# Performance work log

Measured on AMD Instinct MI355X. Metric: run time of the kernel, lower is better.

The kernel has to match this reference:

```python
import jax, jax.numpy as jnp
import numpy as np

N, D, E = 50000, 128, 100000
H1, H2, H3 = 8, 8, 4
NEG_SLOPE = 0.2  # PyG GATv2Conv default negative_slope


def _gatv2_layer(x, src, dst, Wl, Wr, att, b, heads):
    # GATv2Conv(in=D, out=D, heads=heads, concat=False), share_weights=False
    C = Wl.shape[1] // heads
    xl = (x @ Wl).reshape(-1, heads, C)  # source-side transform (x_j)
    xr = (x @ Wr).reshape(-1, heads, C)  # target-side transform (x_i)
    m = jax.nn.leaky_relu(xl[src] + xr[dst], NEG_SLOPE)      # [E,H,C]
    e = jnp.einsum('ehc,hc->eh', m, att)                      # [E,H]
    # segment softmax over incoming edges of each destination node
    emax = jax.ops.segment_max(e, dst, num_segments=N)        # [N,H]
    a = jnp.exp(e - emax[dst])
    denom = jax.ops.segment_sum(a, dst, num_segments=N)       # [N,H] (>0: self-loops)
    a = a / denom[dst]
    out = jax.ops.segment_sum(xl[src] * a[:, :, None], dst, num_segments=N)  # [N,H,C]
    return out.mean(axis=1) + b  # concat=False -> head mean, then bias


def setup_inputs() -> dict:
    key = jax.random.key(0)
    ks = jax.random.split(key, 16)
    x = jax.random.normal(ks[0], (N, D), dtype=jnp.float32)
    src = jax.random.randint(ks[1], (E,), 0, N)
    dst = jax.random.randint(ks[2], (E,), 0, N)
    src = jnp.where(src == dst, (src + 1) % N, src)  # no pre-existing self loops
    edge_index = jnp.stack([src, dst]).astype(jnp.int64)
    s = 1.0 / np.sqrt(D)
    def lin(k, h):
        return jax.random.uniform(k, (D, h * D), jnp.float32, -s, s)
    def attn(k, h):
        return jax.random.uniform(k, (h, D), jnp.float32, -s, s)
    return {
        'x': x, 'edge_index': edge_index,
        'W1l': lin(ks[3], H1), 'W1r': lin(ks[4], H1), 'att1': attn(ks[5], H1), 'b1': jnp.zeros((D,), jnp.float32),
        'W2l': lin(ks[6], H2), 'W2r': lin(ks[7], H2), 'att2': attn(ks[8], H2), 'b2': jnp.zeros((D,), jnp.float32),
        'W3l': lin(ks[9], H3), 'W3r': lin(ks[10], H3), 'att3': attn(ks[11], H3), 'b3': jnp.zeros((D,), jnp.float32),
    }


def reference(x, edge_index, W1l, W1r, att1, b1, W2l, W2r, att2, b2, W3l, W3r, att3, b3):
    # PyG GATv2Conv adds self loops by default
    loops = jnp.arange(N, dtype=edge_index.dtype)
    src = jnp.concatenate([edge_index[0], loops])
    dst = jnp.concatenate([edge_index[1], loops])
    h = x + _gatv2_layer(x, src, dst, W1l, W1r, att1, b1, H1)
    h = jax.nn.elu(h)  # dropout is identity in eval mode
    h = h + _gatv2_layer(h, src, dst, W2l, W2r, att2, b2, H2)
    h = jax.nn.elu(h)
    h = h + _gatv2_layer(h, src, dst, W3l, W3r, att3, b3, H3)
    return h
```

## Files before the change

### kernel.cpp

```cpp
#include <hip/hip_runtime.h>

#define NN 50000
#define DD 128
#define EE 100000
#define ET (EE + NN)

typedef __attribute__((ext_vector_type(4))) float f32x4;
typedef __attribute__((ext_vector_type(8))) short bf16x8;
typedef __attribute__((ext_vector_type(4))) unsigned short u16x4;
typedef __attribute__((ext_vector_type(4))) unsigned int u32x4;
typedef __attribute__((ext_vector_type(2))) unsigned int u32x2;

static __device__ __forceinline__ unsigned short f2bf(float f) {
  union { float f; unsigned int u; } v; v.f = f;
  unsigned int r = (v.u + 0x7FFFu + ((v.u >> 16) & 1u)) >> 16;
  return (unsigned short)r;
}
static __device__ __forceinline__ float bflo(unsigned int u) {
  union { unsigned int u; float f; } v; v.u = u << 16; return v.f;
}
static __device__ __forceinline__ float bfhi(unsigned int u) {
  union { unsigned int u; float f; } v; v.u = u & 0xffff0000u; return v.f;
}

template <int CTRL>
static __device__ __forceinline__ float dpp_add(float x) {
  int xi = __builtin_bit_cast(int, x);
  int yi = __builtin_amdgcn_update_dpp(xi, xi, CTRL, 0xF, 0xF, true);
  return x + __builtin_bit_cast(float, yi);
}
static __device__ __forceinline__ float row16_sum(float p) {
  p = dpp_add<0xB1>(p);
  p = dpp_add<0x4E>(p);
  p = dpp_add<0x141>(p);
  p = dpp_add<0x128>(p);
  return p;
}

__global__ __launch_bounds__(256) void k_prep(
    const float* __restrict__ x, const int* __restrict__ ei,
    const float* __restrict__ W1l, const float* __restrict__ W1r,
    const float* __restrict__ W2l, const float* __restrict__ W2r,
    const float* __restrict__ W3l, const float* __restrict__ W3r,
    const float* __restrict__ att1, const float* __restrict__ att2, const float* __restrict__ att3,
    unsigned short* __restrict__ wt1, unsigned short* __restrict__ wt2,
    unsigned short* __restrict__ wt3,
    float* __restrict__ as1, float* __restrict__ as2, float* __restrict__ as3,
    unsigned short* __restrict__ abf, int* __restrict__ counts) {
  const int i = blockIdx.x * 256 + threadIdx.x;
  const float LOG2E = 1.4426950408889634f;
  if (i < 262144) {
    int half = i >> 17, rem = i & 131071;
    int nn = rem >> 7, k = rem & 127;
    const float* W = half ? W1r : W1l;
    wt1[i] = f2bf(W[(size_t)k * 1024 + nn]);
  } else if (i < 524288) {
    int local = i - 262144;
    int half = local >> 17, rem = local & 131071;
    int nn = rem >> 7, k = rem & 127;
    const float* W = half ? W2r : W2l;
    wt2[local] = f2bf(W[(size_t)k * 1024 + nn]);
  } else if (i < 655360) {
    int local = i - 524288;
    int half = local >> 16, rem = local & 65535;
    int nn = rem >> 7, k = rem & 127;
    const float* W = half ? W3r : W3l;
    wt3[local] = f2bf(W[(size_t)k * 512 + nn]);
  } else if (i < 657920) {
    int local = i - 655360;
    if (local < 1024) as1[local] = att1[local] * LOG2E;
    else if (local < 2048) as2[local - 1024] = att2[local - 1024] * LOG2E;
    else as3[local - 2048] = att3[local - 2048] * LOG2E;
  } else if (i < 807920) {
    int e = i - 657920;
    int dst = (e < EE) ? ei[EE + e] : (e - EE);
    if (dst >= 0 && dst < NN) atomicAdd(&counts[dst], 1);
  } else if (i < 2407920) {
    int u = i - 807920;
    f32x4 v = *(const f32x4*)(x + (size_t)u * 4);
    u16x4 w;
    w.x = f2bf(v.x); w.y = f2bf(v.y); w.z = f2bf(v.z); w.w = f2bf(v.w);
    *(u16x4*)(abf + (size_t)u * 4) = w;
  }
}

__global__ __launch_bounds__(1024) void k_scan(const int* __restrict__ counts,
                                               int* __restrict__ offs,
                                               int* __restrict__ cursor) {
  __shared__ int wsum[16];
  __shared__ int wpre[16];
  __shared__ int wtot;
  const int tid = threadIdx.x;
  const int wv = tid >> 6, lane = tid & 63;
  int carry = 0;
  for (int base = 0; base < NN; base += 4096) {
    int i0 = base + tid * 4;
    int v[4];
#pragma unroll
    for (int q = 0; q < 4; ++q) { int i = i0 + q; v[q] = (i < NN) ? counts[i] : 0; }
    int s = v[0] + v[1] + v[2] + v[3];
    int sc = s;
#pragma unroll
    for (int m = 1; m < 64; m <<= 1) {
      int t = __shfl_up(sc, m, 64);
      if (lane >= m) sc += t;
    }
    if (lane == 63) wsum[wv] = sc;
    __syncthreads();
    if (tid < 16) {
      int t = wsum[tid];
      int scc = t;
#pragma unroll
      for (int m = 1; m < 16; m <<= 1) {
        int u = __shfl_up(scc, m, 64);
        if (tid >= m) scc += u;
      }
      wpre[tid] = scc - t;
      if (tid == 15) wtot = scc;
    }
    __syncthreads();
    int excl = carry + wpre[wv] + (sc - s);
#pragma unroll
    for (int q = 0; q < 4; ++q) {
      int i = i0 + q;
      if (i < NN) { offs[i] = excl; cursor[i] = excl; }
      excl += v[q];
    }
    carry += wtot;
    __syncthreads();
  }
  if (tid == 0) offs[NN] = carry;
}

__global__ void k_fill(const int* __restrict__ ei, int* __restrict__ cursor,
                       int* __restrict__ srcs) {
  int i = blockIdx.x * blockDim.x + threadIdx.x;
  if (i >= ET) return;
  int src, dst;
  if (i < EE) { src = ei[i]; dst = ei[EE + i]; }
  else { src = dst = i - EE; }
  if (dst < 0 || dst >= NN) return;
  if (src < 0 || src >= NN) src = dst;
  int pos = atomicAdd(&cursor[dst], 1);
  if (pos >= 0 && pos < ET) srcs[pos] = src;
}

__global__ __launch_bounds__(256) void gemm_bt(
    const unsigned short* __restrict__ A, const unsigned short* __restrict__ WT,
    unsigned short* __restrict__ Cl, unsigned short* __restrict__ Cr,
    int M, int Nout, int lgny) {
  const int f = blockIdx.x;
  const int c = f & ((1 << lgny) - 1);
  const int x = f >> lgny;
  const int z = c & 1, y = c >> 1;
  const int m0 = x * 128, n0 = y * 128;
  unsigned short* C = z ? Cr : Cl;
  const unsigned short* BT = WT + (size_t)z * Nout * DD;

  __shared__ unsigned short As[128 * 128];
  __shared__ unsigned short Bs[128 * 128];
  const int tid = threadIdx.x;
  const int wave = tid >> 6, lane = tid & 63;
  const int hi = lane >> 4, lr = lane & 15;

#pragma unroll
  for (int i = 0; i < 8; ++i) {
    int row = i * 16 + wave * 4 + hi;
    int c16 = lr ^ (row & 7);
    const unsigned short* ga = A + (size_t)(m0 + row) * DD + c16 * 8;
    __builtin_amdgcn_global_load_lds((const __attribute__((address_space(1))) void*)ga,
        (__attribute__((address_space(3))) void*)(As + i * 2048 + wave * 512), 16, 0, 0);
    const unsigned short* gb = BT + (size_t)(n0 + row) * DD + c16 * 8;
    __builtin_amdgcn_global_load_lds((const __attribute__((address_space(1))) void*)gb,
        (__attribute__((address_space(3))) void*)(Bs + i * 2048 + wave * 512), 16, 0, 0);
  }
  __syncthreads();

  const int wr = (wave >> 1) * 64, wc = (wave & 1) * 64;
  f32x4 acc[4][4];
#pragma unroll
  for (int i = 0; i < 4; ++i)
#pragma unroll
    for (int j = 0; j < 4; ++j) acc[i][j] = (f32x4){0.f, 0.f, 0.f, 0.f};

#pragma unroll
  for (int k0 = 0; k0 < 128; k0 += 32) {
    const int ck = (k0 >> 3) + hi;
    bf16x8 af[4], bfr[4];
#pragma unroll
    for (int mi = 0; mi < 4; ++mi) {
      int r = wr + mi * 16 + lr;
      af[mi] = *(const bf16x8*)&As[r * 128 + ((ck ^ (r & 7)) << 3)];
    }
#pragma unroll
    for (int ni = 0; ni < 4; ++ni) {
      int cc = wc + ni * 16 + lr;
      bfr[ni] = *(const bf16x8*)&Bs[cc * 128 + ((ck ^ (cc & 7)) << 3)];
    }
#pragma unroll
    for (int mi = 0; mi < 4; ++mi)
#pragma unroll
      for (int ni = 0; ni < 4; ++ni)
        acc[mi][ni] = __builtin_amdgcn_mfma_f32_16x16x32_bf16(af[mi], bfr[ni], acc[mi][ni], 0, 0, 0);
  }

#pragma unroll
  for (int mi = 0; mi < 4; ++mi) {
#pragma unroll
    for (int ni = 0; ni < 4; ++ni) {
      int col = n0 + wc + ni * 16 + lr;
#pragma unroll
      for (int j = 0; j < 4; ++j) {
        int row = m0 + wr + mi * 16 + (hi << 2) + j;
        if (row < M) C[(size_t)row * Nout + col] = f2bf(acc[mi][ni][j]);
      }
    }
  }
}

template <int H>
__global__ __launch_bounds__(256) void gat_agg7(
    const unsigned short* __restrict__ xl, const unsigned short* __restrict__ xr,
    const int* __restrict__ offs, const int* __restrict__ srcs,
    const float* __restrict__ att_s,
    const float* __restrict__ bias,
    const float* __restrict__ residf,
    const unsigned short* __restrict__ residb,
    float* __restrict__ outf,
    unsigned short* __restrict__ hbfw,
    int do_elu) {
  constexpr int HG = H / 2;
  constexpr int CPL = 2 * HG;
  constexpr int NW = HG;
  constexpr int LPH = 128 / CPL;
  constexpr int ROW = H * DD;
  constexpr int HALFROW = ROW / 2;
  const int wave = threadIdx.x >> 6, lane = threadIdx.x & 63;
  const int nsub = wave >> 1, g = wave & 1;
  const int cb = g * HALFROW + lane * CPL;
  const int d0 = (lane * CPL) & 127;

  float av[CPL];
#pragma unroll
  for (int c = 0; c < CPL; ++c) av[c] = att_s[cb + c];

  __shared__ float lds[2][2][DD];
  const unsigned short* xl_cb = xl + cb;
  const int stride = gridDim.x * 2;
  int par = 0;

  for (int n = blockIdx.x * 2 + nsub; n < NN; n += stride) {
    const int e0 = offs[n], e1 = offs[n + 1];

    float xrv[CPL];
    {
      const unsigned int* q = (const unsigned int*)(xr + (size_t)n * ROW + cb);
#pragma unroll
      for (int w = 0; w < NW; ++w) {
        unsigned int u = q[w];
        xrv[2 * w] = bflo(u);
        xrv[2 * w + 1] = bfhi(u);
      }
    }
    float acc[CPL];
#pragma unroll
    for (int c = 0; c < CPL; ++c) acc[c] = 0.f;
    float mx = -1e30f, dn = 0.f;

    for (int j = e0; j < e1; j += 4) {
      const int B = (e1 - j < 4) ? (e1 - j) : 4;
      unsigned int rows[4][NW];
#pragma unroll
      for (int b = 0; b < 4; ++b) {
        if (b < B) {
          int s = srcs[j + b];
          const unsigned int* qq = (const unsigned int*)(xl_cb + (size_t)s * ROW);
#pragma unroll
          for (int w = 0; w < NW; ++w) rows[b][w] = qq[w];
        }
      }
      float p[4];
#pragma unroll
      for (int b = 0; b < 4; ++b) {
        float pp = -1e30f;
        if (b < B) {
          pp = 0.f;
#pragma unroll
          for (int w = 0; w < NW; ++w) {
            float x0 = bflo(rows[b][w]), x1 = bfhi(rows[b][w]);
            float z0 = x0 + xrv[2 * w]; z0 = fmaxf(z0, 0.2f * z0);
            float z1 = x1 + xrv[2 * w + 1]; z1 = fmaxf(z1, 0.2f * z1);
            pp = fmaf(z0, av[2 * w], pp);
            pp = fmaf(z1, av[2 * w + 1], pp);
          }
          pp = row16_sum(pp);
          if constexpr (LPH == 32) pp += __shfl_xor(pp, 16, 64);
        }
        p[b] = pp;
      }
      float pm = fmaxf(fmaxf(p[0], p[1]), fmaxf(p[2], p[3]));
      if (__any(pm > mx + 11.5f)) {
        float mnew = fmaxf(mx, pm);
        float sc = __builtin_amdgcn_exp2f(mx - mnew);
        dn *= sc;
#pragma unroll
        for (int c = 0; c < CPL; ++c) acc[c] *= sc;
        mx = mnew;
      }
#pragma unroll
      for (int b = 0; b < 4; ++b) {
        if (b < B) {
          float wt = __builtin_amdgcn_exp2f(p[b] - mx);
          dn += wt;
#pragma unroll
          for (int w = 0; w < NW; ++w) {
            acc[2 * w] = fmaf(wt, bflo(rows[b][w]), acc[2 * w]);
            acc[2 * w + 1] = fmaf(wt, bfhi(rows[b][w]), acc[2 * w + 1]);
          }
        }
      }
    }

    float r[CPL];
    const float inv = (1.f / (float)H) / dn;
#pragma unroll
    for (int c = 0; c < CPL; ++c) r[c] = acc[c] * inv;
#pragma unroll
    for (int m = LPH; m < 64; m <<= 1)
#pragma unroll
      for (int c = 0; c < CPL; ++c) r[c] += __shfl_xor(r[c], m, 64);

    if (g == 1 && lane < LPH) {
#pragma unroll
      for (int c = 0; c < CPL; ++c) lds[par][nsub][d0 + c] = r[c];
    }
    __syncthreads();
    if (g == 0 && lane < LPH) {
      float rv[CPL];
      if (residf) {
#pragma unroll
        for (int c = 0; c < CPL; c += 4) {
          f32x4 v = *(const f32x4*)(residf + (size_t)n * DD + d0 + c);
          rv[c] = v.x; rv[c + 1] = v.y; rv[c + 2] = v.z; rv[c + 3] = v.w;
        }
      } else {
        const unsigned int* q = (const unsigned int*)(residb + (size_t)n * DD + d0);
#pragma unroll
        for (int w = 0; w < CPL / 2; ++w) {
          unsigned int u = q[w];
          rv[2 * w] = bflo(u);
          rv[2 * w + 1] = bfhi(u);
        }
      }
      float o[CPL];
#pragma unroll
      for (int c = 0; c < CPL; ++c) {
        o[c] = r[c] + lds[par][nsub][d0 + c] + bias[d0 + c] + rv[c];
        if (do_elu && o[c] < 0.f)
          o[c] = __builtin_amdgcn_exp2f(o[c] * 1.4426950408889634f) - 1.f;
      }
      if (outf) {
#pragma unroll
        for (int c = 0; c < CPL; c += 4) {
          f32x4 v; v.x = o[c]; v.y = o[c + 1]; v.z = o[c + 2]; v.w = o[c + 3];
          *(f32x4*)(outf + (size_t)n * DD + d0 + c) = v;
        }
      }
      if (hbfw) {
        unsigned int pk[CPL / 2];
#pragma unroll
        for (int q = 0; q < CPL / 2; ++q)
          pk[q] = (unsigned int)f2bf(o[2 * q]) | ((unsigned int)f2bf(o[2 * q + 1]) << 16);
        if constexpr (CPL == 8) {
          u32x4 v; v.x = pk[0]; v.y = pk[1]; v.z = pk[2]; v.w = pk[3];
          *(u32x4*)(hbfw + (size_t)n * DD + d0) = v;
        } else {
          u32x2 v; v.x = pk[0]; v.y = pk[1];
          *(u32x2*)(hbfw + (size_t)n * DD + d0) = v;
        }
      }
    }
    par ^= 1;
  }
}

extern "C" void kernel_launch(void* const* d_in, const int* in_sizes, int n_in,
                              void* d_out, int out_size, void* d_ws, size_t ws_size,
                              hipStream_t stream) {
  const float* x = (const float*)d_in[0];
  const int* ei = (const int*)d_in[1];
  const float* W1l = (const float*)d_in[2];
  const float* W1r = (const float*)d_in[3];
  const float* att1 = (const float*)d_in[4];
  const float* b1 = (const float*)d_in[5];
  const float* W2l = (const float*)d_in[6];
  const float* W2r = (const float*)d_in[7];
  const float* att2 = (const float*)d_in[8];
  const float* b2 = (const float*)d_in[9];
  const float* W3l = (const float*)d_in[10];
  const float* W3r = (const float*)d_in[11];
  const float* att3 = (const float*)d_in[12];
  const float* b3 = (const float*)d_in[13];
  float* out = (float*)d_out;

  char* p = (char*)d_ws;
  auto carve = [&](size_t bytes) {
    char* r = p;
    p += (bytes + 255) & ~(size_t)255;
    return r;
  };
  unsigned short* xl = (unsigned short*)carve((size_t)NN * 1024 * 2);
  unsigned short* xr = (unsigned short*)carve((size_t)NN * 1024 * 2);
  unsigned short* abf = (unsigned short*)carve((size_t)NN * DD * 2);
  unsigned short* wt1 = (unsigned short*)carve((size_t)2 * 1024 * DD * 2);
  unsigned short* wt2 = (unsigned short*)carve((size_t)2 * 1024 * DD * 2);
  unsigned short* wt3 = (unsigned short*)carve((size_t)2 * 512 * DD * 2);
  float* as1 = (float*)carve((size_t)8 * DD * 4);
  float* as2 = (float*)carve((size_t)8 * DD * 4);
  float* as3 = (float*)carve((size_t)4 * DD * 4);
  int* counts = (int*)carve((size_t)NN * 4);
  int* offs = (int*)carve(((size_t)NN + 1) * 4);
  int* cursor = (int*)carve((size_t)NN * 4);
  int* srcs = (int*)carve((size_t)ET * 4);
  size_t needed = (size_t)(p - (char*)d_ws);
  if (needed > ws_size) return;

  hipMemsetAsync(counts, 0, (size_t)NN * 4, stream);
  k_prep<<<9406, 256, 0, stream>>>(x, ei, W1l, W1r, W2l, W2r, W3l, W3r, att1, att2, att3,
                                   wt1, wt2, wt3, as1, as2, as3, abf, counts);
  k_scan<<<1, 1024, 0, stream>>>(counts, offs, cursor);
  k_fill<<<(ET + 255) / 256, 256, 0, stream>>>(ei, cursor, srcs);

  const int gx = (NN + 127) / 128;
  const int ga = 2048;
  gemm_bt<<<gx * 16, 256, 0, stream>>>(abf, wt1, xl, xr, NN, 1024, 4);
  gat_agg7<8><<<ga, 256, 0, stream>>>(xl, xr, offs, srcs, as1, b1, x, nullptr,
                                      nullptr, abf, 1);
  gemm_bt<<<gx * 16, 256, 0, stream>>>(abf, wt2, xl, xr, NN, 1024, 4);
  gat_agg7<8><<<ga, 256, 0, stream>>>(xl, xr, offs, srcs, as2, b2, nullptr, abf,
                                      nullptr, abf, 1);
  gemm_bt<<<gx * 8, 256, 0, stream>>>(abf, wt3, xl, xr, NN, 512, 3);
  gat_agg7<4><<<ga, 256, 0, stream>>>(xl, xr, offs, srcs, as3, b3, nullptr, abf,
                                      out, nullptr, 0);
}
```

Before: 534.7 us.

## Launch one block per node pair in aggregation and swizzle GEMM blocks across XCDs

The aggregation kernel drops its persistent grid-stride loop and launches one block per pair of destination nodes. This removes the per-iteration block-wide barrier coupling between nodes and the double-buffered shared array, and spreads uneven edge counts across more blocks. Per-lane gathers of xl, xr and the residual are now single 64/128-bit vector loads. The GEMM remaps blockIdx so neighbouring tiles land on the same XCD, to improve L2 reuse of the A and weight tiles. The cost is many more small blocks to launch and schedule, and the remap assumes the grid size is divisible by 8.

```diff
diff --git a/kernel.cpp b/kernel.cpp
--- a/kernel.cpp
+++ b/kernel.cpp
@@ -149,7 +149,7 @@
     const unsigned short* __restrict__ A, const unsigned short* __restrict__ WT,
     unsigned short* __restrict__ Cl, unsigned short* __restrict__ Cr,
     int M, int Nout, int lgny) {
-  const int f = blockIdx.x;
+  const int f = (blockIdx.x & 7) * (gridDim.x >> 3) + (blockIdx.x >> 3);
   const int c = f & ((1 << lgny) - 1);
   const int x = f >> lgny;
   const int z = c & 1, y = c >> 1;
@@ -219,7 +219,7 @@
 }
 
 template <int H>
-__global__ __launch_bounds__(256) void gat_agg7(
+__global__ __launch_bounds__(256) void gat_agg8(
     const unsigned short* __restrict__ xl, const unsigned short* __restrict__ xr,
     const int* __restrict__ offs, const int* __restrict__ srcs,
     const float* __restrict__ att_s,
@@ -237,150 +237,160 @@
   constexpr int HALFROW = ROW / 2;
   const int wave = threadIdx.x >> 6, lane = threadIdx.x & 63;
   const int nsub = wave >> 1, g = wave & 1;
+  const int n = blockIdx.x * 2 + nsub;
+  if (n >= NN) return;
   const int cb = g * HALFROW + lane * CPL;
   const int d0 = (lane * CPL) & 127;
 
-  float av[CPL];
-#pragma unroll
-  for (int c = 0; c < CPL; ++c) av[c] = att_s[cb + c];
-
-  __shared__ float lds[2][2][DD];
+  float xrv[CPL], av[CPL];
+  {
+    unsigned int uw[NW];
+    if constexpr (NW == 4) {
+      u32x4 v = *(const u32x4*)(xr + (size_t)n * ROW + cb);
+      uw[0] = v.x; uw[1] = v.y; uw[2] = v.z; uw[3] = v.w;
+    } else {
+      u32x2 v = *(const u32x2*)(xr + (size_t)n * ROW + cb);
+      uw[0] = v.x; uw[1] = v.y;
+    }
+#pragma unroll
+    for (int w = 0; w < NW; ++w) {
+      xrv[2 * w] = bflo(uw[w]);
+      xrv[2 * w + 1] = bfhi(uw[w]);
+    }
+#pragma unroll
+    for (int c = 0; c < CPL; ++c) av[c] = att_s[cb + c];
+  }
+
+  float acc[CPL];
+#pragma unroll
+  for (int c = 0; c < CPL; ++c) acc[c] = 0.f;
+  float mx = -1e30f, dn = 0.f;
+
+  const int e0 = offs[n], e1 = offs[n + 1];
   const unsigned short* xl_cb = xl + cb;
-  const int stride = gridDim.x * 2;
-  int par = 0;
-
-  for (int n = blockIdx.x * 2 + nsub; n < NN; n += stride) {
-    const int e0 = offs[n], e1 = offs[n + 1];
-
-    float xrv[CPL];
-    {
-      const unsigned int* q = (const unsigned int*)(xr + (size_t)n * ROW + cb);
-#pragma unroll
-      for (int w = 0; w < NW; ++w) {
-        unsigned int u = q[w];
-        xrv[2 * w] = bflo(u);
-        xrv[2 * w + 1] = bfhi(u);
-      }
-    }
-    float acc[CPL];
-#pragma unroll
-    for (int c = 0; c < CPL; ++c) acc[c] = 0.f;
-    float mx = -1e30f, dn = 0.f;
-
-    for (int j = e0; j < e1; j += 4) {
-      const int B = (e1 - j < 4) ? (e1 - j) : 4;
-      unsigned int rows[4][NW];
-#pragma unroll
-      for (int b = 0; b < 4; ++b) {
-        if (b < B) {
-          int s = srcs[j + b];
-          const unsigned int* qq = (const unsigned int*)(xl_cb + (size_t)s * ROW);
-#pragma unroll
-          for (int w = 0; w < NW; ++w) rows[b][w] = qq[w];
+  for (int j = e0; j < e1; j += 4) {
+    const int B = (e1 - j < 4) ? (e1 - j) : 4;
+    unsigned int rows[4][NW];
+#pragma unroll
+    for (int b = 0; b < 4; ++b) {
+      if (b < B) {
+        int s = srcs[j + b];
+        if constexpr (NW == 4) {
+          u32x4 v = *(const u32x4*)(xl_cb + (size_t)s * ROW);
+          rows[b][0] = v.x; rows[b][1] = v.y; rows[b][2] = v.z; rows[b][3] = v.w;
+        } else {
+          u32x2 v = *(const u32x2*)(xl_cb + (size_t)s * ROW);
+          rows[b][0] = v.x; rows[b][1] = v.y;
         }
       }
-      float p[4];
-#pragma unroll
-      for (int b = 0; b < 4; ++b) {
-        float pp = -1e30f;
-        if (b < B) {
-          pp = 0.f;
-#pragma unroll
-          for (int w = 0; w < NW; ++w) {
-            float x0 = bflo(rows[b][w]), x1 = bfhi(rows[b][w]);
-            float z0 = x0 + xrv[2 * w]; z0 = fmaxf(z0, 0.2f * z0);
-            float z1 = x1 + xrv[2 * w + 1]; z1 = fmaxf(z1, 0.2f * z1);
-            pp = fmaf(z0, av[2 * w], pp);
-            pp = fmaf(z1, av[2 * w + 1], pp);
-          }
-          pp = row16_sum(pp);
-          if constexpr (LPH == 32) pp += __shfl_xor(pp, 16, 64);
+    }
+    float p[4];
+#pragma unroll
+    for (int b = 0; b < 4; ++b) {
+      float pp = -1e30f;
+      if (b < B) {
+        pp = 0.f;
+#pragma unroll
+        for (int w = 0; w < NW; ++w) {
+          float x0 = bflo(rows[b][w]), x1 = bfhi(rows[b][w]);
+          float z0 = x0 + xrv[2 * w]; z0 = fmaxf(z0, 0.2f * z0);
+          float z1 = x1 + xrv[2 * w + 1]; z1 = fmaxf(z1, 0.2f * z1);
+          pp = fmaf(z0, av[2 * w], pp);
+          pp = fmaf(z1, av[2 * w + 1], pp);
         }
-        p[b] = pp;
-      }
-      float pm = fmaxf(fmaxf(p[0], p[1]), fmaxf(p[2], p[3]));
-      if (__any(pm > mx + 11.5f)) {
-        float mnew = fmaxf(mx, pm);
-        float sc = __builtin_amdgcn_exp2f(mx - mnew);
-        dn *= sc;
-#pragma unroll
-        for (int c = 0; c < CPL; ++c) acc[c] *= sc;
-        mx = mnew;
-      }
-#pragma unroll
-      for (int b = 0; b < 4; ++b) {
-        if (b < B) {
-          float wt = __builtin_amdgcn_exp2f(p[b] - mx);
-          dn += wt;
-#pragma unroll
-          for (int w = 0; w < NW; ++w) {
-            acc[2 * w] = fmaf(wt, bflo(rows[b][w]), acc[2 * w]);
-            acc[2 * w + 1] = fmaf(wt, bfhi(rows[b][w]), acc[2 * w + 1]);
-          }
+        pp = row16_sum(pp);
+        if constexpr (LPH == 32) pp += __shfl_xor(pp, 16, 64);
+      }
+      p[b] = pp;
+    }
+    float pm = fmaxf(fmaxf(p[0], p[1]), fmaxf(p[2], p[3]));
+    if (__any(pm > mx + 11.5f)) {
+      float mnew = fmaxf(mx, pm);
+      float sc = __builtin_amdgcn_exp2f(mx - mnew);
+      dn *= sc;
+#pragma unroll
+      for (int c = 0; c < CPL; ++c) acc[c] *= sc;
+      mx = mnew;
+    }
+#pragma unroll
+    for (int b = 0; b < 4; ++b) {
+      if (b < B) {
+        float wt = __builtin_amdgcn_exp2f(p[b] - mx);
+        dn += wt;
+#pragma unroll
+        for (int w = 0; w < NW; ++w) {
+          acc[2 * w] = fmaf(wt, bflo(rows[b][w]), acc[2 * w]);
+          acc[2 * w + 1] = fmaf(wt, bfhi(rows[b][w]), acc[2 * w + 1]);
         }
       }
     }
-
-    float r[CPL];
-    const float inv = (1.f / (float)H) / dn;
-#pragma unroll
-    for (int c = 0; c < CPL; ++c) r[c] = acc[c] * inv;
-#pragma unroll
-    for (int m = LPH; m < 64; m <<= 1)
-#pragma unroll
-      for (int c = 0; c < CPL; ++c) r[c] += __shfl_xor(r[c], m, 64);
-
-    if (g == 1 && lane < LPH) {
-#pragma unroll
-      for (int c = 0; c < CPL; ++c) lds[par][nsub][d0 + c] = r[c];
-    }
-    __syncthreads();
-    if (g == 0 && lane < LPH) {
-      float rv[CPL];
-      if (residf) {
-#pragma unroll
-        for (int c = 0; c < CPL; c += 4) {
-          f32x4 v = *(const f32x4*)(residf + (size_t)n * DD + d0 + c);
-          rv[c] = v.x; rv[c + 1] = v.y; rv[c + 2] = v.z; rv[c + 3] = v.w;
-        }
+  }
+
+  float r[CPL];
+  const float inv = (1.f / (float)H) / dn;
+#pragma unroll
+  for (int c = 0; c < CPL; ++c) r[c] = acc[c] * inv;
+#pragma unroll
+  for (int m = LPH; m < 64; m <<= 1)
+#pragma unroll
+    for (int c = 0; c < CPL; ++c) r[c] += __shfl_xor(r[c], m, 64);
+
+  __shared__ float lds[2][DD];
+  if (g == 1 && lane < LPH) {
+#pragma unroll
+    for (int c = 0; c < CPL; ++c) lds[nsub][d0 + c] = r[c];
+  }
+  __syncthreads();
+  if (g == 0 && lane < LPH) {
+    float rv[CPL];
+    if (residf) {
+#pragma unroll
+      for (int c = 0; c < CPL; c += 4) {
+        f32x4 v = *(const f32x4*)(residf + (size_t)n * DD + d0 + c);
+        rv[c] = v.x; rv[c + 1] = v.y; rv[c + 2] = v.z; rv[c + 3] = v.w;
+      }
+    } else {
+      unsigned int uw[CPL / 2];
+      if constexpr (CPL == 8) {
+        u32x4 v = *(const u32x4*)(residb + (size_t)n * DD + d0);
+        uw[0] = v.x; uw[1] = v.y; uw[2] = v.z; uw[3] = v.w;
       } else {
-        const unsigned int* q = (const unsigned int*)(residb + (size_t)n * DD + d0);
-#pragma unroll
-        for (int w = 0; w < CPL / 2; ++w) {
-          unsigned int u = q[w];
-          rv[2 * w] = bflo(u);
-          rv[2 * w + 1] = bfhi(u);
-        }
-      }
-      float o[CPL];
-#pragma unroll
-      for (int c = 0; c < CPL; ++c) {
-        o[c] = r[c] + lds[par][nsub][d0 + c] + bias[d0 + c] + rv[c];
-        if (do_elu && o[c] < 0.f)
-          o[c] = __builtin_amdgcn_exp2f(o[c] * 1.4426950408889634f) - 1.f;
-      }
-      if (outf) {
-#pragma unroll
-        for (int c = 0; c < CPL; c += 4) {
-          f32x4 v; v.x = o[c]; v.y = o[c + 1]; v.z = o[c + 2]; v.w = o[c + 3];
-          *(f32x4*)(outf + (size_t)n * DD + d0 + c) = v;
-        }
-      }
-      if (hbfw) {
-        unsigned int pk[CPL / 2];
-#pragma unroll
-        for (int q = 0; q < CPL / 2; ++q)
-          pk[q] = (unsigned int)f2bf(o[2 * q]) | ((unsigned int)f2bf(o[2 * q + 1]) << 16);
-        if constexpr (CPL == 8) {
-          u32x4 v; v.x = pk[0]; v.y = pk[1]; v.z = pk[2]; v.w = pk[3];
-          *(u32x4*)(hbfw + (size_t)n * DD + d0) = v;
-        } else {
-          u32x2 v; v.x = pk[0]; v.y = pk[1];
-          *(u32x2*)(hbfw + (size_t)n * DD + d0) = v;
-        }
-      }
-    }
-    par ^= 1;
+        u32x2 v = *(const u32x2*)(residb + (size_t)n * DD + d0);
+        uw[0] = v.x; uw[1] = v.y;
+      }
+#pragma unroll
+      for (int w = 0; w < CPL / 2; ++w) {
+        rv[2 * w] = bflo(uw[w]);
+        rv[2 * w + 1] = bfhi(uw[w]);
+      }
+    }
+    float o[CPL];
+#pragma unroll
+    for (int c = 0; c < CPL; ++c) {
+      o[c] = r[c] + lds[nsub][d0 + c] + bias[d0 + c] + rv[c];
+      if (do_elu && o[c] < 0.f)
+        o[c] = __builtin_amdgcn_exp2f(o[c] * 1.4426950408889634f) - 1.f;
+    }
+    if (outf) {
+#pragma unroll
+      for (int c = 0; c < CPL; c += 4) {
+        f32x4 v; v.x = o[c]; v.y = o[c + 1]; v.z = o[c + 2]; v.w = o[c + 3];
+        *(f32x4*)(outf + (size_t)n * DD + d0 + c) = v;
+      }
+    }
+    if (hbfw) {
+      unsigned int pk[CPL / 2];
+#pragma unroll
+      for (int q = 0; q < CPL / 2; ++q)
+        pk[q] = (unsigned int)f2bf(o[2 * q]) | ((unsigned int)f2bf(o[2 * q + 1]) << 16);
+      if constexpr (CPL == 8) {
+        u32x4 v; v.x = pk[0]; v.y = pk[1]; v.z = pk[2]; v.w = pk[3];
+        *(u32x4*)(hbfw + (size_t)n * DD + d0) = v;
+      } else {
+        u32x2 v; v.x = pk[0]; v.y = pk[1];
+        *(u32x2*)(hbfw + (size_t)n * DD + d0) = v;
+      }
+    }
   }
 }
 
@@ -432,14 +442,14 @@
   k_fill<<<(ET + 255) / 256, 256, 0, stream>>>(ei, cursor, srcs);
 
   const int gx = (NN + 127) / 128;
-  const int ga = 2048;
+  const int ga = (NN + 1) / 2;
   gemm_bt<<<gx * 16, 256, 0, stream>>>(abf, wt1, xl, xr, NN, 1024, 4);
-  gat_agg7<8><<<ga, 256, 0, stream>>>(xl, xr, offs, srcs, as1, b1, x, nullptr,
+  gat_agg8<8><<<ga, 256, 0, stream>>>(xl, xr, offs, srcs, as1, b1, x, nullptr,
                                       nullptr, abf, 1);
   gemm_bt<<<gx * 16, 256, 0, stream>>>(abf, wt2, xl, xr, NN, 1024, 4);
-  gat_agg7<8><<<ga, 256, 0, stream>>>(xl, xr, offs, srcs, as2, b2, nullptr, abf,
+  gat_agg8<8><<<ga, 256, 0, stream>>>(xl, xr, offs, srcs, as2, b2, nullptr, abf,
                                       nullptr, abf, 1);
   gemm_bt<<<gx * 8, 256, 0, stream>>>(abf, wt3, xl, xr, NN, 512, 3);
-  gat_agg7<4><<<ga, 256, 0, stream>>>(xl, xr, offs, srcs, as3, b3, nullptr, abf,
+  gat_agg8<4><<<ga, 256, 0, stream>>>(xl, xr, offs, srcs, as3, b3, nullptr, abf,
                                       out, nullptr, 0);
 }
```

New measurement: 451.9 us. 15.5% less time.
